# Kernel tuning notes

Measured on AMD Instinct MI355X. Metric: run time of the kernel, lower is better.

## Reference

```python
import jax, jax.numpy as jnp
import numpy as np

EPS = 1e-8
FUSION_THRESHOLD = 0.95
N, D = 8192, 256
NUM_CATEGORIES = 80


def setup_inputs() -> dict:
    key = jax.random.key(0)
    k1, k2, k3 = jax.random.split(key, 3)
    return {
        "kernels": jax.random.normal(k1, (1, N, D), dtype=jnp.float32),
        "categories": jax.random.randint(k2, (1, N), 0, NUM_CATEGORIES, dtype=jnp.int64),
        "scores": jax.random.uniform(k3, (1, N), dtype=jnp.float32),
    }


def reference(kernels, categories, scores):
    # squeeze batch (module asserts batch == 1)
    k = kernels[0]          # [N, D]
    c = categories[0]       # [N]
    s = scores[0]           # [N]

    # CosineSelfSimilarity: normalize rows (norm computed in float32, clamped at eps)
    nrm = jnp.maximum(
        jnp.linalg.norm(k.astype(jnp.float32), axis=1, keepdims=True), EPS
    )
    a_norm = k / nrm
    sim = a_norm @ a_norm.T                                  # [N, N]

    # upper-triangular threshold mask (diagonal included, matches torch.triu)
    label = jnp.triu(sim) >= FUSION_THRESHOLD
    # category gating (mask_categories=True)
    label = label & (c[:, None] == c[None, :])

    # greedy cumsum dedup: a kernel survives iff its column has < 2 hits so far
    cum = jnp.cumsum(label.astype(jnp.float32), axis=0) < 2.0  # [N, N] bool
    keep = jnp.diagonal(cum)                                   # [N] bool

    # In the original, rows are boolean-selected by `keep` (dynamic shape).
    # For jit compatibility we keep shape [N] and zero out dropped rows.
    label_f = (label & cum & keep[:, None]).astype(jnp.float32)  # [N, N]
    label_norm = jnp.sum(label_f, axis=1, keepdims=True)          # [N, 1]
    # kept rows always include the diagonal => norm >= 1; clamp for dropped rows
    fused = (label_f @ k) / jnp.maximum(label_norm, 1.0)          # [N, D]

    cats_out = jnp.where(keep, c, -1)
    scores_out = jnp.where(keep, s, 0.0)
    return fused[None], cats_out[None], scores_out[None], keep[None]
```

## Files before the change

### kernel.cpp

```cpp
#include <hip/hip_runtime.h>
#include <cstdint>

#define NROWS 8192
#define DDIM  256
#define THR   0.95f
#define EPSN  1e-8f
#define IMAX  0x7FFFFFFF
#define NCAT  80
#define MAXT  16

typedef unsigned short u16;
typedef short v8s __attribute__((ext_vector_type(8)));
typedef float v4f __attribute__((ext_vector_type(4)));

__device__ __forceinline__ u16 f2b(float f) {
    union { float f; unsigned int i; } v; v.f = f;
    if ((v.i & 0x7F800000u) == 0x7F800000u) {
        return (u16)((v.i >> 16) | ((v.i & 0xFFFFu) ? 0x40 : 0));
    }
    unsigned int r = v.i + 0x7FFFu + ((v.i >> 16) & 1u);
    return (u16)(r >> 16);
}

__global__ __launch_bounds__(256) void k_norm_sort(const float* __restrict__ kin,
                                                   const int* __restrict__ cat,
                                                   u16* __restrict__ anorm,
                                                   int* __restrict__ sortedRows,
                                                   int* __restrict__ catBase,
                                                   int* __restrict__ mergeCnt) {
    const int t = threadIdx.x;
    if (blockIdx.x < NROWS / 4) {
        const int w = t >> 6, l = t & 63;
        const int row = (blockIdx.x << 2) + w;
        const float4 v = ((const float4*)(kin + (size_t)row * DDIM))[l];
        float s = v.x * v.x + v.y * v.y + v.z * v.z + v.w * v.w;
        for (int o = 32; o >= 1; o >>= 1) s += __shfl_xor(s, o);
        const float rn = 1.0f / fmaxf(sqrtf(s), EPSN);
        ushort4 o4;
        o4.x = f2b(v.x * rn); o4.y = f2b(v.y * rn);
        o4.z = f2b(v.z * rn); o4.w = f2b(v.w * rn);
        ((ushort4*)(anorm + (size_t)row * DDIM))[l] = o4;
        return;
    }
    __shared__ u16 h[NCAT][256];
    __shared__ int tot[NCAT];
    __shared__ int base[NCAT + 1];
    for (int i = t; i < NCAT * 256; i += 256) ((u16*)h)[i] = 0;
    __syncthreads();
    {
        const int r0 = t << 5;
        for (int k = 0; k < 32; ++k) h[cat[r0 + k]][t]++;
    }
    __syncthreads();
    if (t < NCAT) {
        int s = 0;
        for (int q = 0; q < 256; ++q) s += (int)h[t][q];
        tot[t] = s;
    }
    __syncthreads();
    if (t == 0) {
        int run = 0;
        for (int c = 0; c < NCAT; ++c) { base[c] = run; run += tot[c]; }
        base[NCAT] = run;
        *mergeCnt = 0;
    }
    __syncthreads();
    if (t <= NCAT) catBase[t] = base[t];
    if (t < NCAT) {
        int run = 0;
        for (int q = 0; q < 256; ++q) { const int v = (int)h[t][q]; h[t][q] = (u16)run; run += v; }
    }
    __syncthreads();
    {
        const int r0 = t << 5;
        for (int k = 0; k < 32; ++k) {
            const int r = r0 + k, c = cat[r];
            const int rel = (int)h[c][t]++;
            sortedRows[base[c] + rel] = r;
        }
    }
}

__global__ __launch_bounds__(256) void k_hits_cat(const u16* __restrict__ anorm,
                                                  const float* __restrict__ sc,
                                                  const int* __restrict__ sortedRows,
                                                  const int* __restrict__ catBase,
                                                  int* __restrict__ hit1,
                                                  int* __restrict__ hit2,
                                                  int* __restrict__ mergeCnt,
                                                  int* __restrict__ mergeList,
                                                  float* __restrict__ out) {
    const int c  = blockIdx.x >> 4;
    const int ct = blockIdx.x & 15;
    const int nbase = catBase[c];
    const int nc = catBase[c + 1] - nbase;
    const int ncT = (nc + 15) >> 4;
    if (ct >= ncT) return;
    const int* lst = sortedRows + nbase;

    __shared__ int colH1[16];
    const int t = threadIdx.x;
    if (t < 16) colH1[t] = IMAX;
    __syncthreads();

    const int wv = t >> 6, l = t & 63;
    const int lo16 = l & 15, quad = l >> 4;

    const int qloc = (ct << 4) + lo16;
    const int gq = lst[qloc < nc ? qloc : nc - 1];
    const u16* qrow = anorm + ((size_t)gq << 8) + (quad << 3);
    v8s bfr[8];
#pragma unroll
    for (int kk = 0; kk < 8; ++kk) bfr[kk] = *(const v8s*)(qrow + (kk << 5));

    for (int rt = wv; rt <= ct; rt += 4) {
        const int ploc = (rt << 4) + lo16;
        const int gp = lst[ploc < nc ? ploc : nc - 1];
        const u16* prow = anorm + ((size_t)gp << 8) + (quad << 3);
        v4f acc = {0.f, 0.f, 0.f, 0.f};
#pragma unroll
        for (int kk = 0; kk < 8; ++kk) {
            const v8s af = *(const v8s*)(prow + (kk << 5));
            acc = __builtin_amdgcn_mfma_f32_16x16x32_bf16(af, bfr[kk], acc, 0, 0, 0);
        }
#pragma unroll
        for (int reg = 0; reg < 4; ++reg) {
            const int p = (rt << 4) + (quad << 2) + reg;
            if (acc[reg] >= THR && p < qloc && qloc < nc) atomicMin(&colH1[lo16], p);
        }
    }
    __syncthreads();

    if (t < 16) {
        const int q = (ct << 4) + t;
        if (q < nc) {
            const int g = lst[q];
            const int h1p = colH1[t];
            const bool hasHit = (h1p != IMAX);
            hit1[g] = hasHit ? lst[h1p] : g;
            hit2[g] = hasHit ? 0 : IMAX;
            float* cats  = out + (size_t)NROWS * DDIM;
            float* scso  = cats + NROWS;
            float* keepo = scso + NROWS;
            cats[g]  = hasHit ? -1.0f : (float)c;
            scso[g]  = hasHit ? 0.0f : sc[g];
            keepo[g] = hasHit ? 0.0f : 1.0f;
            if (hasHit) mergeList[atomicAdd(mergeCnt, 1)] = g;
        }
    }
}

__global__ __launch_bounds__(256) void k_out(const float* __restrict__ kin,
                                             const int* __restrict__ hit1,
                                             const int* __restrict__ hit2,
                                             const int* __restrict__ mergeCnt,
                                             const int* __restrict__ mergeList,
                                             float* __restrict__ out) {
    const int t = threadIdx.x, l = t & 63;
    const int i = (int)(blockIdx.x << 2) + (t >> 6);
    const bool keep = (hit2[i] == IMAX);

    float ax = 0.f, ay = 0.f, az = 0.f, aw = 0.f;
    if (keep) {
        const float4 v = ((const float4*)(kin + (size_t)i * DDIM))[l];
        ax = v.x; ay = v.y; az = v.z; aw = v.w;
        int cnt = 1;
        const int mc = *mergeCnt;
        for (int q = 0; q < mc; q++) {
            const int jr = mergeList[q];
            if (hit1[jr] == i) {
                const float4 b = ((const float4*)(kin + (size_t)jr * DDIM))[l];
                ax += b.x; ay += b.y; az += b.z; aw += b.w; cnt++;
            }
        }
        const float fc = (float)cnt;
        ax /= fc; ay /= fc; az /= fc; aw /= fc;
    }
    float4 o4; o4.x = ax; o4.y = ay; o4.z = az; o4.w = aw;
    ((float4*)(out + (size_t)i * DDIM))[l] = o4;
}

extern "C" void kernel_launch(void* const* d_in, const int* in_sizes, int n_in,
                              void* d_out, int out_size, void* d_ws, size_t ws_size,
                              hipStream_t stream) {
    (void)in_sizes; (void)n_in; (void)out_size; (void)ws_size;
    const float* kin = (const float*)d_in[0];
    const int*   cat = (const int*)d_in[1];
    const float* sc  = (const float*)d_in[2];
    float* out = (float*)d_out;

    char* ws = (char*)d_ws;
    u16* anorm      = (u16*)ws;
    int* hit1       = (int*)(ws + (size_t)NROWS * DDIM * 2);
    int* hit2       = hit1 + NROWS;
    int* sortedRows = hit2 + NROWS;
    int* catBase    = sortedRows + NROWS;
    int* mergeCnt   = catBase + 128;
    int* mergeList  = mergeCnt + 16;

    k_norm_sort<<<NROWS / 4 + 1, 256, 0, stream>>>(kin, cat, anorm, sortedRows,
                                                   catBase, mergeCnt);
    k_hits_cat<<<NCAT * MAXT, 256, 0, stream>>>(anorm, sc, sortedRows, catBase,
                                                hit1, hit2, mergeCnt, mergeList, out);
    k_out<<<NROWS / 4, 256, 0, stream>>>(kin, hit1, hit2, mergeCnt, mergeList, out);
}
```

Before: 95.00 us.

## Fuse output kernel into norm pass and per-category last-block merge fixup

The standalone output kernel is removed. The normalization kernel now writes each input row directly to the output as the default fused result. In the similarity kernel, the last block to finish each category, detected with an atomic per-category counter, zeroes the merged rows and recomputes averages only for the rows that absorbed others. This saves a kernel launch and the per-row scan over a global merge list, at the cost of a threadfence/atomic completion protocol and a serial fixup inside one block per category.

```diff
diff --git a/kernel.cpp b/kernel.cpp
--- a/kernel.cpp
+++ b/kernel.cpp
@@ -27,12 +27,14 @@
                                                    u16* __restrict__ anorm,
                                                    int* __restrict__ sortedRows,
                                                    int* __restrict__ catBase,
-                                                   int* __restrict__ mergeCnt) {
+                                                   int* __restrict__ catDone,
+                                                   float* __restrict__ out) {
     const int t = threadIdx.x;
     if (blockIdx.x < NROWS / 4) {
         const int w = t >> 6, l = t & 63;
         const int row = (blockIdx.x << 2) + w;
         const float4 v = ((const float4*)(kin + (size_t)row * DDIM))[l];
+        ((float4*)(out + (size_t)row * DDIM))[l] = v;
         float s = v.x * v.x + v.y * v.y + v.z * v.z + v.w * v.w;
         for (int o = 32; o >= 1; o >>= 1) s += __shfl_xor(s, o);
         const float rn = 1.0f / fmaxf(sqrtf(s), EPSN);
@@ -45,6 +47,7 @@
     __shared__ u16 h[NCAT][256];
     __shared__ int tot[NCAT];
     __shared__ int base[NCAT + 1];
+    if (t < NCAT) catDone[t] = 0;
     for (int i = t; i < NCAT * 256; i += 256) ((u16*)h)[i] = 0;
     __syncthreads();
     {
@@ -62,7 +65,6 @@
         int run = 0;
         for (int c = 0; c < NCAT; ++c) { base[c] = run; run += tot[c]; }
         base[NCAT] = run;
-        *mergeCnt = 0;
     }
     __syncthreads();
     if (t <= NCAT) catBase[t] = base[t];
@@ -81,14 +83,14 @@
     }
 }
 
-__global__ __launch_bounds__(256) void k_hits_cat(const u16* __restrict__ anorm,
+__global__ __launch_bounds__(256) void k_hits_cat(const float* __restrict__ kin,
+                                                  const u16* __restrict__ anorm,
                                                   const float* __restrict__ sc,
                                                   const int* __restrict__ sortedRows,
                                                   const int* __restrict__ catBase,
+                                                  int* __restrict__ catDone,
                                                   int* __restrict__ hit1,
                                                   int* __restrict__ hit2,
-                                                  int* __restrict__ mergeCnt,
-                                                  int* __restrict__ mergeList,
                                                   float* __restrict__ out) {
     const int c  = blockIdx.x >> 4;
     const int ct = blockIdx.x & 15;
@@ -99,6 +101,10 @@
     const int* lst = sortedRows + nbase;
 
     __shared__ int colH1[16];
+    __shared__ int mlist[256];
+    __shared__ int mtgt[256];
+    __shared__ int mn;
+    __shared__ int lastFlag;
     const int t = threadIdx.x;
     if (t < 16) colH1[t] = IMAX;
     __syncthreads();
@@ -145,39 +151,42 @@
             cats[g]  = hasHit ? -1.0f : (float)c;
             scso[g]  = hasHit ? 0.0f : sc[g];
             keepo[g] = hasHit ? 0.0f : 1.0f;
-            if (hasHit) mergeList[atomicAdd(mergeCnt, 1)] = g;
-        }
-    }
-}
-
-__global__ __launch_bounds__(256) void k_out(const float* __restrict__ kin,
-                                             const int* __restrict__ hit1,
-                                             const int* __restrict__ hit2,
-                                             const int* __restrict__ mergeCnt,
-                                             const int* __restrict__ mergeList,
-                                             float* __restrict__ out) {
-    const int t = threadIdx.x, l = t & 63;
-    const int i = (int)(blockIdx.x << 2) + (t >> 6);
-    const bool keep = (hit2[i] == IMAX);
-
-    float ax = 0.f, ay = 0.f, az = 0.f, aw = 0.f;
-    if (keep) {
-        const float4 v = ((const float4*)(kin + (size_t)i * DDIM))[l];
-        ax = v.x; ay = v.y; az = v.z; aw = v.w;
+        }
+    }
+    __threadfence();
+    __syncthreads();
+    if (t == 0) {
+        lastFlag = (atomicAdd(&catDone[c], 1) == ncT - 1);
+        mn = 0;
+    }
+    __syncthreads();
+    if (!lastFlag) return;
+    __threadfence();
+
+    for (int q = t; q < nc; q += 256) {
+        const int g = lst[q];
+        if (hit2[g] != IMAX) {
+            const int j = atomicAdd(&mn, 1);
+            mlist[j] = g;
+            mtgt[j] = hit1[g];
+        }
+    }
+    __syncthreads();
+    const int m = mn;
+    for (int j = 0; j < m; ++j)
+        out[(size_t)mlist[j] * DDIM + t] = 0.f;
+    for (int j = 0; j < m; ++j) {
+        const int i = mtgt[j];
+        if (hit2[i] != IMAX) continue;
+        bool first = true;
+        for (int p = 0; p < j; ++p) if (mtgt[p] == i) { first = false; break; }
+        if (!first) continue;
+        float acc = kin[(size_t)i * DDIM + t];
         int cnt = 1;
-        const int mc = *mergeCnt;
-        for (int q = 0; q < mc; q++) {
-            const int jr = mergeList[q];
-            if (hit1[jr] == i) {
-                const float4 b = ((const float4*)(kin + (size_t)jr * DDIM))[l];
-                ax += b.x; ay += b.y; az += b.z; aw += b.w; cnt++;
-            }
-        }
-        const float fc = (float)cnt;
-        ax /= fc; ay /= fc; az /= fc; aw /= fc;
-    }
-    float4 o4; o4.x = ax; o4.y = ay; o4.z = az; o4.w = aw;
-    ((float4*)(out + (size_t)i * DDIM))[l] = o4;
+        for (int p = 0; p < m; ++p)
+            if (mtgt[p] == i) { acc += kin[(size_t)mlist[p] * DDIM + t]; cnt++; }
+        out[(size_t)i * DDIM + t] = acc / (float)cnt;
+    }
 }
 
 extern "C" void kernel_launch(void* const* d_in, const int* in_sizes, int n_in,
@@ -195,12 +204,10 @@
     int* hit2       = hit1 + NROWS;
     int* sortedRows = hit2 + NROWS;
     int* catBase    = sortedRows + NROWS;
-    int* mergeCnt   = catBase + 128;
-    int* mergeList  = mergeCnt + 16;
+    int* catDone    = catBase + 128;
 
     k_norm_sort<<<NROWS / 4 + 1, 256, 0, stream>>>(kin, cat, anorm, sortedRows,
-                                                   catBase, mergeCnt);
-    k_hits_cat<<<NCAT * MAXT, 256, 0, stream>>>(anorm, sc, sortedRows, catBase,
-                                                hit1, hit2, mergeCnt, mergeList, out);
-    k_out<<<NROWS / 4, 256, 0, stream>>>(kin, hit1, hit2, mergeCnt, mergeList, out);
-}
+                                                   catBase, catDone, out);
+    k_hits_cat<<<NCAT * MAXT, 256, 0, stream>>>(kin, anorm, sc, sortedRows, catBase,
+                                                catDone, hit1, hit2, out);
+}
```

Result: slower. 172.7 us (+81.8%).

## Copy input rows into output during normalization and patch only merged rows

Applied to the files above, without the earlier changes.

The normalization kernel now writes each input row straight to the fused output, so the default case (an unmerged row equals itself) needs no later pass. The hits kernel zeroes rows that were marked dropped, and a single-block fix-up kernel averages rows only for targets that received merges. This removes the full 8 MB read-and-write pass of the old output kernel. The trade-off is a serial single-block loop over the merge list, which becomes slow if many rows merge.

```diff
diff --git a/kernel.cpp b/kernel.cpp
--- a/kernel.cpp
+++ b/kernel.cpp
@@ -27,12 +27,14 @@
                                                    u16* __restrict__ anorm,
                                                    int* __restrict__ sortedRows,
                                                    int* __restrict__ catBase,
-                                                   int* __restrict__ mergeCnt) {
+                                                   int* __restrict__ mergeCnt,
+                                                   float* __restrict__ out) {
     const int t = threadIdx.x;
     if (blockIdx.x < NROWS / 4) {
         const int w = t >> 6, l = t & 63;
         const int row = (blockIdx.x << 2) + w;
         const float4 v = ((const float4*)(kin + (size_t)row * DDIM))[l];
+        ((float4*)(out + (size_t)row * DDIM))[l] = v;
         float s = v.x * v.x + v.y * v.y + v.z * v.z + v.w * v.w;
         for (int o = 32; o >= 1; o >>= 1) s += __shfl_xor(s, o);
         const float rn = 1.0f / fmaxf(sqrtf(s), EPSN);
@@ -148,36 +150,38 @@
             if (hasHit) mergeList[atomicAdd(mergeCnt, 1)] = g;
         }
     }
-}
-
-__global__ __launch_bounds__(256) void k_out(const float* __restrict__ kin,
+    for (int q = 0; q < 16; ++q) {
+        const int qq = (ct << 4) + q;
+        if (qq < nc && colH1[q] != IMAX) {
+            const int g = lst[qq];
+            out[(size_t)g * DDIM + t] = 0.f;
+        }
+    }
+}
+
+__global__ __launch_bounds__(256) void k_fix(const float* __restrict__ kin,
                                              const int* __restrict__ hit1,
                                              const int* __restrict__ hit2,
                                              const int* __restrict__ mergeCnt,
                                              const int* __restrict__ mergeList,
                                              float* __restrict__ out) {
-    const int t = threadIdx.x, l = t & 63;
-    const int i = (int)(blockIdx.x << 2) + (t >> 6);
-    const bool keep = (hit2[i] == IMAX);
-
-    float ax = 0.f, ay = 0.f, az = 0.f, aw = 0.f;
-    if (keep) {
-        const float4 v = ((const float4*)(kin + (size_t)i * DDIM))[l];
-        ax = v.x; ay = v.y; az = v.z; aw = v.w;
+    const int mc = *mergeCnt;
+    if (mc == 0) return;
+    const int t = threadIdx.x;
+    for (int j = 0; j < mc; ++j) {
+        const int i = hit1[mergeList[j]];
+        if (hit2[i] != IMAX) continue;
+        bool first = true;
+        for (int p = 0; p < j; ++p) if (hit1[mergeList[p]] == i) { first = false; break; }
+        if (!first) continue;
+        float acc = kin[(size_t)i * DDIM + t];
         int cnt = 1;
-        const int mc = *mergeCnt;
-        for (int q = 0; q < mc; q++) {
-            const int jr = mergeList[q];
-            if (hit1[jr] == i) {
-                const float4 b = ((const float4*)(kin + (size_t)jr * DDIM))[l];
-                ax += b.x; ay += b.y; az += b.z; aw += b.w; cnt++;
-            }
-        }
-        const float fc = (float)cnt;
-        ax /= fc; ay /= fc; az /= fc; aw /= fc;
-    }
-    float4 o4; o4.x = ax; o4.y = ay; o4.z = az; o4.w = aw;
-    ((float4*)(out + (size_t)i * DDIM))[l] = o4;
+        for (int p = 0; p < mc; ++p) {
+            const int jr = mergeList[p];
+            if (hit1[jr] == i) { acc += kin[(size_t)jr * DDIM + t]; cnt++; }
+        }
+        out[(size_t)i * DDIM + t] = acc / (float)cnt;
+    }
 }
 
 extern "C" void kernel_launch(void* const* d_in, const int* in_sizes, int n_in,
@@ -199,8 +203,8 @@
     int* mergeList  = mergeCnt + 16;
 
     k_norm_sort<<<NROWS / 4 + 1, 256, 0, stream>>>(kin, cat, anorm, sortedRows,
-                                                   catBase, mergeCnt);
+                                                   catBase, mergeCnt, out);
     k_hits_cat<<<NCAT * MAXT, 256, 0, stream>>>(anorm, sc, sortedRows, catBase,
                                                 hit1, hit2, mergeCnt, mergeList, out);
-    k_out<<<NROWS / 4, 256, 0, stream>>>(kin, hit1, hit2, mergeCnt, mergeList, out);
-}
+    k_fix<<<1, 256, 0, stream>>>(kin, hit1, hit2, mergeCnt, mergeList, out);
+}
```

Result: no change. 94.32 us (-0.7%).
